# Kernel optimization log

Measured on AMD Instinct MI355X. Metric: run time of the kernel, lower is better.

## Reference

```python
import jax, jax.numpy as jnp
import numpy as np

EMBED = 1024
HEAD = 64
BLOCK = 2048
B = 8


def setup_inputs() -> dict:
    key = jax.random.key(0)
    k1, k2, k3, k4 = jax.random.split(key, 4)
    inputs = jax.random.normal(k1, (B, BLOCK, EMBED), dtype=jnp.float32)
    s = 1.0 / np.sqrt(EMBED)
    Wk = jax.random.normal(k2, (EMBED, HEAD), dtype=jnp.float32) * s
    Wq = jax.random.normal(k3, (EMBED, HEAD), dtype=jnp.float32) * s
    Wv = jax.random.normal(k4, (EMBED, HEAD), dtype=jnp.float32) * s
    return {"inputs": inputs, "Wk": Wk, "Wq": Wq, "Wv": Wv}


def reference(inputs, Wk, Wq, Wv):
    # inputs: [B, T, E]; projections (bias-free Linear)
    k = inputs @ Wk  # [B, T, H]
    q = inputs @ Wq  # [B, T, H]
    v = inputs @ Wv  # [B, T, H]
    # Faithful to source: wei = k @ q^T (NOT q @ k^T)
    wei = jnp.einsum("bth,bsh->bts", k, q) * (HEAD ** -0.5)  # [B, T, T]
    T = inputs.shape[1]
    causal = jnp.tril(jnp.ones((T, T), dtype=bool))
    wei = jnp.where(causal, wei, -jnp.inf)
    wei = jax.nn.softmax(wei, axis=-1)
    out = jnp.einsum("bts,bsh->bth", wei, v)  # [B, T, H]
    return out
```

## Files before the change

### kernel.cpp

```cpp
#include <hip/hip_runtime.h>
#include <hip/hip_bf16.h>
#include <stdint.h>


typedef __attribute__((ext_vector_type(4))) float f32x4;
typedef __attribute__((ext_vector_type(4))) short s16x4;
typedef __attribute__((ext_vector_type(8))) short s16x8;
typedef __attribute__((ext_vector_type(2))) unsigned int u32x2;
typedef __attribute__((ext_vector_type(4))) unsigned int u32x4;

__device__ __forceinline__ unsigned bf16pack(float a, float b){
    unsigned ua = __builtin_bit_cast(unsigned, a);
    unsigned ub = __builtin_bit_cast(unsigned, b);
    return ((ua + 0x8000u) >> 16) | ((ub + 0x8000u) & 0xffff0000u);
}
__device__ __forceinline__ unsigned short bf16one(float a){
    return (unsigned short)((__builtin_bit_cast(unsigned, a) + 0x8000u) >> 16);
}
__device__ __forceinline__ void gload16(const void* g, unsigned short* l){
    __builtin_amdgcn_global_load_lds((const __attribute__((address_space(1))) unsigned int*)g,
                                     (__attribute__((address_space(3))) unsigned int*)l, 16, 0, 0);
}

__global__ __launch_bounds__(256) void wprep_kernel(const float* __restrict__ Wk,
                                                    const float* __restrict__ Wq,
                                                    const float* __restrict__ Wv,
                                                    unsigned short* __restrict__ WT){
    __shared__ float lw[1024][8];
    int w = blockIdx.x, n0 = blockIdx.y * 8, tid = threadIdx.x;
    const float* src = (w == 0) ? Wk : (w == 1) ? Wq : Wv;
    float scale = (w == 0) ? 0.18033688011112042f : 1.0f;
    for (int it = 0; it < 8; ++it){
        int idx = it * 256 + tid;
        int k = idx >> 1, half = idx & 1;
        f32x4 v = *(const f32x4*)(src + k * 64 + n0 + half * 4);
        *(f32x4*)&lw[k][half * 4] = v;
    }
    __syncthreads();
    int n = tid >> 5, kc = (tid & 31) * 32;
    unsigned short* dst = WT + (size_t)((w * 64 + n0 + n) * 1024 + kc);
    #pragma unroll
    for (int c = 0; c < 4; c++){
        s16x8 v;
        #pragma unroll
        for (int e = 0; e < 8; e++)
            v[e] = (short)bf16one(lw[kc + c * 8 + e][n] * scale);
        *(s16x8*)(dst + c * 8) = v;
    }
}

__global__ __launch_bounds__(256) void proj_kernel(const float* __restrict__ x,
                                                   const unsigned short* __restrict__ WT,
                                                   unsigned short* __restrict__ kb,
                                                   unsigned short* __restrict__ qb,
                                                   unsigned short* __restrict__ vT){
    __shared__ unsigned short smem[32768];
    int tid = threadIdx.x; int l = tid & 63; int w = tid >> 6;
    int lr = l & 15, lg = l >> 4;
    int row0 = blockIdx.x * 32;
    int b = row0 >> 11, t0 = row0 & 2047;
    const float* xbase = x + (size_t)row0 * 1024;

    auto stage = [&](int k0, int buf){
        #pragma unroll
        for (int t = 0; t < 2; t++){
            int i = w * 2 + t;
            int r = i * 4 + (l >> 4);
            int c = l & 15;
            gload16(xbase + (size_t)r * 1024 + k0 + ((c ^ ((r & 7) << 1)) * 4),
                    smem + buf * 4096 + i * 512);
        }
        #pragma unroll
        for (int u = 0; u < 6; u++){
            int i = w * 6 + u;
            int r = i * 8 + (l >> 3);
            int c = l & 7;
            gload16(WT + (size_t)r * 1024 + k0 + ((c ^ (r & 7)) * 8),
                    smem + 8192 + buf * 12288 + i * 512);
        }
    };

    f32x4 acc[2][3] = {};
    stage(0, 0);
    __syncthreads();
    int cur = 0;
    for (int k0 = 0; k0 < 1024; k0 += 64){
        int kn = (k0 + 64 < 1024) ? (k0 + 64) : 960;
        stage(kn, cur ^ 1);
        s16x8 af[2][2];
        #pragma unroll
        for (int mf = 0; mf < 2; mf++){
            int r = mf * 16 + lr;
            const unsigned short* xrow = smem + cur * 4096 + r * 128;
            #pragma unroll
            for (int kc = 0; kc < 2; kc++){
                int c0 = (kc * 8 + lg * 2) ^ ((r & 7) << 1);
                f32x4 v0 = *(const f32x4*)(xrow + c0 * 8);
                f32x4 v1 = *(const f32x4*)(xrow + c0 * 8 + 8);
                u32x4 pk;
                pk[0] = bf16pack(v0[0], v0[1]); pk[1] = bf16pack(v0[2], v0[3]);
                pk[2] = bf16pack(v1[0], v1[1]); pk[3] = bf16pack(v1[2], v1[3]);
                af[mf][kc] = __builtin_bit_cast(s16x8, pk);
            }
        }
        #pragma unroll
        for (int nn = 0; nn < 3; nn++){
            int r = (w * 3 + nn) * 16 + lr;
            const unsigned short* wrow = smem + 8192 + cur * 12288 + r * 64;
            s16x8 b0 = *(const s16x8*)(wrow + ((lg       ^ (r & 7)) * 8));
            s16x8 b1 = *(const s16x8*)(wrow + (((4 + lg) ^ (r & 7)) * 8));
            acc[0][nn] = __builtin_amdgcn_mfma_f32_16x16x32_bf16(af[0][0], b0, acc[0][nn], 0, 0, 0);
            acc[0][nn] = __builtin_amdgcn_mfma_f32_16x16x32_bf16(af[0][1], b1, acc[0][nn], 0, 0, 0);
            acc[1][nn] = __builtin_amdgcn_mfma_f32_16x16x32_bf16(af[1][0], b0, acc[1][nn], 0, 0, 0);
            acc[1][nn] = __builtin_amdgcn_mfma_f32_16x16x32_bf16(af[1][1], b1, acc[1][nn], 0, 0, 0);
        }
        __syncthreads();
        cur ^= 1;
    }
    #pragma unroll
    for (int mf = 0; mf < 2; mf++)
        #pragma unroll
        for (int nn = 0; nn < 3; nn++){
            int col = (w * 3 + nn) * 16 + lr;
            int row = mf * 16 + lg * 4;
            #pragma unroll
            for (int r = 0; r < 4; r++)
                smem[(row + r) * 200 + col] = bf16one(acc[mf][nn][r]);
        }
    __syncthreads();
    {
        int r2 = tid >> 3, c2 = (tid & 7) * 16;
        const unsigned short* srowp = smem + r2 * 200 + c2;
        unsigned short* dst = (c2 < 64)
            ? kb + (size_t)(b * 2048 + t0 + r2) * 64 + c2
            : qb + (size_t)(b * 2048 + t0 + r2) * 64 + (c2 - 64);
        *(s16x8*)(dst)     = *(const s16x8*)(srowp);
        *(s16x8*)(dst + 8) = *(const s16x8*)(srowp + 8);
        int h = tid >> 2, q3 = tid & 3;
        s16x8 vv;
        #pragma unroll
        for (int e = 0; e < 8; e++)
            vv[e] = smem[(q3 * 8 + e) * 200 + 128 + h];
        *(s16x8*)(vT + (size_t)(b * 64 + h) * 2048 + t0 + q3 * 8) = vv;
    }
}

template<int NS>
__global__ __launch_bounds__(256) void attn_part_kernel(const unsigned short* __restrict__ kb,
                                                        const unsigned short* __restrict__ qb,
                                                        const unsigned short* __restrict__ vT,
                                                        float* __restrict__ out,
                                                        float* __restrict__ accp,
                                                        float* __restrict__ ml){
    __shared__ unsigned short Klds[2][64 * 64];
    __shared__ unsigned short Vlds[2][64 * 64];
    int tid = threadIdx.x; int l = tid & 63; int w = tid >> 6;
    int lr = l & 15, lg = l >> 4;
    int bx = blockIdx.x;
    int b = bx & 7;
    int r9 = bx >> 3;
    int bt = 31 - (r9 / NS);
    int strip = r9 % NS;
    int t0 = bt * 64;
    int tw = t0 + w * 16;
    const unsigned short* fqp = kb + (size_t)(b * 2048 + tw + lr) * 64 + lg * 8;
    s16x8 fq0 = *(const s16x8*)(fqp);
    s16x8 fq1 = *(const s16x8*)(fqp + 32);
    const unsigned short* qbb = qb + (size_t)b * 2048 * 64;
    const unsigned short* vbb = vT + (size_t)b * 64 * 2048;

    int srhi = l >> 3;
    int schk = l & 7;
    f32x4 acc[4] = {};
    float mrun = -3.0e38f, lrun = 0.0f;

    {
        int s0 = strip * 64;
        #pragma unroll
        for (int t = 0; t < 2; t++){
            int ti = w * 2 + t;
            int row = ti * 8 + srhi;
            gload16(qbb + (size_t)(s0 + row) * 64 + ((schk ^ (row & 7)) * 8), &Klds[0][ti * 512]);
            gload16(vbb + (size_t)row * 2048 + s0 + ((schk ^ (row & 7)) * 8), &Vlds[0][ti * 512]);
        }
    }
    __syncthreads();
    int cur = 0;
    for (int c = strip; c <= bt; c += NS){
        int nc = (c + NS <= bt) ? (c + NS) : c;
        int ns0 = nc * 64;
        #pragma unroll
        for (int t = 0; t < 2; t++){
            int ti = w * 2 + t;
            int row = ti * 8 + srhi;
            gload16(qbb + (size_t)(ns0 + row) * 64 + ((schk ^ (row & 7)) * 8), &Klds[cur ^ 1][ti * 512]);
            gload16(vbb + (size_t)row * 2048 + ns0 + ((schk ^ (row & 7)) * 8), &Vlds[cur ^ 1][ti * 512]);
        }
        f32x4 Cs[4];
        #pragma unroll
        for (int n = 0; n < 4; n++){
            int r = n * 16 + lr;
            const unsigned short* ka = &Klds[cur][r * 64];
            s16x8 k0 = *(const s16x8*)(ka + ((lg       ^ (r & 7)) * 8));
            s16x8 k1 = *(const s16x8*)(ka + (((4 + lg) ^ (r & 7)) * 8));
            f32x4 z = {};
            z     = __builtin_amdgcn_mfma_f32_16x16x32_bf16(k0, fq0, z, 0, 0, 0);
            Cs[n] = __builtin_amdgcn_mfma_f32_16x16x32_bf16(k1, fq1, z, 0, 0, 0);
        }
        if (c == bt){
            #pragma unroll
            for (int n = 0; n < 4; n++)
                #pragma unroll
                for (int r = 0; r < 4; r++)
                    if (n * 16 + lg * 4 + r > w * 16 + lr) Cs[n][r] = -3.0e38f;
        }
        float pm = -3.0e38f;
        #pragma unroll
        for (int n = 0; n < 4; n++)
            #pragma unroll
            for (int r = 0; r < 4; r++) pm = fmaxf(pm, Cs[n][r]);
        pm = fmaxf(pm, __shfl_xor(pm, 16));
        pm = fmaxf(pm, __shfl_xor(pm, 32));
        float mnew = fmaxf(mrun, pm);
        float scl = exp2f(mrun - mnew);
        float p[4][4]; float ps = 0.0f;
        #pragma unroll
        for (int n = 0; n < 4; n++)
            #pragma unroll
            for (int r = 0; r < 4; r++){ float e = exp2f(Cs[n][r] - mnew); p[n][r] = e; ps += e; }
        ps += __shfl_xor(ps, 16);
        ps += __shfl_xor(ps, 32);
        lrun = lrun * scl + ps;
        mrun = mnew;
        #pragma unroll
        for (int h16 = 0; h16 < 4; h16++) acc[h16] *= scl;
        s16x4 pb[4];
        #pragma unroll
        for (int n = 0; n < 4; n++){
            u32x2 t; t[0] = bf16pack(p[n][0], p[n][1]); t[1] = bf16pack(p[n][2], p[n][3]);
            pb[n] = __builtin_bit_cast(s16x4, t);
        }
        #pragma unroll
        for (int h16 = 0; h16 < 4; h16++){
            int r = h16 * 16 + lr;
            const unsigned short* va = &Vlds[cur][r * 64];
            #pragma unroll
            for (int sl = 0; sl < 4; sl++){
                s16x4 fv = *(const s16x4*)(va + (((sl * 2 + (lg >> 1)) ^ (r & 7)) * 8) + (lg & 1) * 4);
                acc[h16] = __builtin_amdgcn_mfma_f32_16x16x16bf16_1k(fv, pb[sl], acc[h16], 0, 0, 0);
            }
        }
        __syncthreads();
        cur ^= 1;
    }
    float* accdst = (strip == 0) ? out : (accp + (size_t)(strip - 1) * (8 * 2048 * 64));
    #pragma unroll
    for (int h16 = 0; h16 < 4; h16++)
        *(f32x4*)(accdst + (size_t)(b * 2048 + tw + lr) * 64 + h16 * 16 + lg * 4) = acc[h16];
    if (lg == 0){
        int idx = ((strip * 8 + b) * 32 + bt) * 64 + w * 16 + lr;
        ml[idx * 2]     = mrun;
        ml[idx * 2 + 1] = lrun;
    }
}

template<int NS>
__global__ __launch_bounds__(256) void attn_merge_kernel(const float* __restrict__ accp,
                                                         const float* __restrict__ ml,
                                                         float* __restrict__ out){
    int bt = blockIdx.x, b = blockIdx.y;
    int tid = threadIdx.x;
    int row = tid >> 2, cg = (tid & 3) * 16;
    float m[NS], lv[NS];
    float mg = -3.0e38f;
    #pragma unroll
    for (int s = 0; s < NS; s++){
        int idx = (((s * 8 + b) * 32 + bt) * 64 + row) * 2;
        m[s] = ml[idx]; lv[s] = ml[idx + 1];
        mg = fmaxf(mg, m[s]);
    }
    float wt[NS]; float lt = 0.0f;
    #pragma unroll
    for (int s = 0; s < NS; s++){ wt[s] = exp2f(m[s] - mg); lt += lv[s] * wt[s]; }
    float inv = 1.0f / lt;
    size_t base = (size_t)(b * 2048 + bt * 64 + row) * 64 + cg;
    #pragma unroll
    for (int g = 0; g < 4; g++){
        f32x4 o = (*(const f32x4*)(out + base + g * 4)) * wt[0];
        #pragma unroll
        for (int s = 1; s < NS; s++)
            o += (*(const f32x4*)(accp + (size_t)(s - 1) * (8 * 2048 * 64) + base + g * 4)) * wt[s];
        o *= inv;
        *(f32x4*)(out + base + g * 4) = o;
    }
}

__global__ __launch_bounds__(256) void attn_kernel(const unsigned short* __restrict__ kb,
                                                   const unsigned short* __restrict__ qb,
                                                   const unsigned short* __restrict__ vT,
                                                   float* __restrict__ out){
    __shared__ unsigned short Klds[2][64 * 64];
    __shared__ unsigned short Vlds[2][64 * 64];
    int tid = threadIdx.x; int l = tid & 63; int w = tid >> 6;
    int lr = l & 15, lg = l >> 4;
    int bx = blockIdx.x;
    int b = bx & 7;
    int bt = bx >> 3;
    int t0 = bt * 64;
    int tw = t0 + w * 16;
    const unsigned short* fqp = kb + (size_t)(b * 2048 + tw + lr) * 64 + lg * 8;
    s16x8 fq0 = *(const s16x8*)(fqp);
    s16x8 fq1 = *(const s16x8*)(fqp + 32);
    const unsigned short* qbb = qb + (size_t)b * 2048 * 64;
    const unsigned short* vbb = vT + (size_t)b * 64 * 2048;
    int srhi = l >> 3;
    int schk = l & 7;
    f32x4 acc[4] = {};
    float mrun = -3.0e38f, lrun = 0.0f;
    #pragma unroll
    for (int t = 0; t < 2; t++){
        int ti = w * 2 + t;
        int row = ti * 8 + srhi;
        gload16(qbb + (size_t)row * 64 + ((schk ^ (row & 7)) * 8), &Klds[0][ti * 512]);
        gload16(vbb + (size_t)row * 2048 + ((schk ^ (row & 7)) * 8), &Vlds[0][ti * 512]);
    }
    __syncthreads();
    int cur = 0;
    for (int c = 0; c <= bt; ++c){
        int nc = (c + 1 <= bt) ? (c + 1) : bt;
        int ns0 = nc * 64;
        #pragma unroll
        for (int t = 0; t < 2; t++){
            int ti = w * 2 + t;
            int row = ti * 8 + srhi;
            gload16(qbb + (size_t)(ns0 + row) * 64 + ((schk ^ (row & 7)) * 8), &Klds[cur ^ 1][ti * 512]);
            gload16(vbb + (size_t)row * 2048 + ns0 + ((schk ^ (row & 7)) * 8), &Vlds[cur ^ 1][ti * 512]);
        }
        f32x4 Cs[4];
        #pragma unroll
        for (int n = 0; n < 4; n++){
            int r = n * 16 + lr;
            const unsigned short* ka = &Klds[cur][r * 64];
            s16x8 k0 = *(const s16x8*)(ka + ((lg       ^ (r & 7)) * 8));
            s16x8 k1 = *(const s16x8*)(ka + (((4 + lg) ^ (r & 7)) * 8));
            f32x4 z = {};
            z     = __builtin_amdgcn_mfma_f32_16x16x32_bf16(k0, fq0, z, 0, 0, 0);
            Cs[n] = __builtin_amdgcn_mfma_f32_16x16x32_bf16(k1, fq1, z, 0, 0, 0);
        }
        if (c == bt){
            #pragma unroll
            for (int n = 0; n < 4; n++)
                #pragma unroll
                for (int r = 0; r < 4; r++)
                    if (n * 16 + lg * 4 + r > w * 16 + lr) Cs[n][r] = -3.0e38f;
        }
        float pm = -3.0e38f;
        #pragma unroll
        for (int n = 0; n < 4; n++)
            #pragma unroll
            for (int r = 0; r < 4; r++) pm = fmaxf(pm, Cs[n][r]);
        pm = fmaxf(pm, __shfl_xor(pm, 16));
        pm = fmaxf(pm, __shfl_xor(pm, 32));
        float mnew = fmaxf(mrun, pm);
        float scl = exp2f(mrun - mnew);
        float p[4][4]; float ps = 0.0f;
        #pragma unroll
        for (int n = 0; n < 4; n++)
            #pragma unroll
            for (int r = 0; r < 4; r++){ float e = exp2f(Cs[n][r] - mnew); p[n][r] = e; ps += e; }
        ps += __shfl_xor(ps, 16);
        ps += __shfl_xor(ps, 32);
        lrun = lrun * scl + ps;
        mrun = mnew;
        #pragma unroll
        for (int h16 = 0; h16 < 4; h16++) acc[h16] *= scl;
        s16x4 pb[4];
        #pragma unroll
        for (int n = 0; n < 4; n++){
            u32x2 t; t[0] = bf16pack(p[n][0], p[n][1]); t[1] = bf16pack(p[n][2], p[n][3]);
            pb[n] = __builtin_bit_cast(s16x4, t);
        }
        #pragma unroll
        for (int h16 = 0; h16 < 4; h16++){
            int r = h16 * 16 + lr;
            const unsigned short* va = &Vlds[cur][r * 64];
            #pragma unroll
            for (int sl = 0; sl < 4; sl++){
                s16x4 fv = *(const s16x4*)(va + (((sl * 2 + (lg >> 1)) ^ (r & 7)) * 8) + (lg & 1) * 4);
                acc[h16] = __builtin_amdgcn_mfma_f32_16x16x16bf16_1k(fv, pb[sl], acc[h16], 0, 0, 0);
            }
        }
        __syncthreads();
        cur ^= 1;
    }
    float inv = 1.0f / lrun;
    #pragma unroll
    for (int h16 = 0; h16 < 4; h16++){
        f32x4 o = acc[h16] * inv;
        *(f32x4*)(out + (size_t)(b * 2048 + tw + lr) * 64 + h16 * 16 + lg * 4) = o;
    }
}

extern "C" void kernel_launch(void* const* d_in, const int* in_sizes, int n_in,
                              void* d_out, int out_size, void* d_ws, size_t ws_size,
                              hipStream_t stream) {
    const float* x  = (const float*)d_in[0];
    const float* Wk = (const float*)d_in[1];
    const float* Wq = (const float*)d_in[2];
    const float* Wv = (const float*)d_in[3];
    float* out = (float*)d_out;
    char* ws = (char*)d_ws;
    if (ws_size < (size_t)7 * 1024 * 1024) return;
    unsigned short* WT = (unsigned short*)(ws);
    unsigned short* kb = (unsigned short*)(ws + (1u << 20));
    unsigned short* qb = (unsigned short*)(ws + (3u << 20));
    unsigned short* vT = (unsigned short*)(ws + (5u << 20));
    hipLaunchKernelGGL(wprep_kernel, dim3(3, 8), dim3(256), 0, stream, Wk, Wq, Wv, WT);
    hipLaunchKernelGGL(proj_kernel, dim3(512), dim3(256), 0, stream, x, WT, kb, qb, vT);
    if (ws_size >= (size_t)20 * 1024 * 1024){
        float* accp = (float*)(ws + ((size_t)7 << 20));
        float* ml   = (float*)(ws + ((size_t)19 << 20));
        hipLaunchKernelGGL((attn_part_kernel<4>), dim3(1024), dim3(256), 0, stream,
                           kb, qb, vT, out, accp, ml);
        hipLaunchKernelGGL((attn_merge_kernel<4>), dim3(32, 8), dim3(256), 0, stream,
                           accp, ml, out);
    } else if (ws_size >= (size_t)12 * 1024 * 1024){
        float* accp = (float*)(ws + ((size_t)7 << 20));
        float* ml   = (float*)(ws + ((size_t)11 << 20));
        hipLaunchKernelGGL((attn_part_kernel<2>), dim3(512), dim3(256), 0, stream,
                           kb, qb, vT, out, accp, ml);
        hipLaunchKernelGGL((attn_merge_kernel<2>), dim3(32, 8), dim3(256), 0, stream,
                           accp, ml, out);
    } else {
        hipLaunchKernelGGL(attn_kernel, dim3(256), dim3(256), 0, stream, kb, qb, vT, out);
    }
}
```

Measured before the change: 50.21 us.

## Enlarge projection tile to 64 rows and stage x as pre-packed bf16

The projection kernel now uses 512-thread blocks over 64 rows, half as many blocks, so each staged W tile is reused across twice as many rows. Each wave handles one 16-row slice and half of the 192 output columns. The x tile is no longer copied as fp32 through global_load_lds. Each thread loads 8 floats into registers during the current k-step, converts them to bf16, and writes them into the other LDS buffer. This cuts x LDS traffic and moves the bf16 conversion out of the MFMA loop. The cost is a register round trip on the x loads that is only partly overlapped, and fewer blocks (256) to fill the GPU.

After: 53.02 us. 5.6% more time.

```diff
diff --git a/kernel.cpp b/kernel.cpp
--- a/kernel.cpp
+++ b/kernel.cpp
@@ -49,7 +49,7 @@
     }
 }
 
-__global__ __launch_bounds__(256) void proj_kernel(const float* __restrict__ x,
+__global__ __launch_bounds__(512) void proj_kernel(const float* __restrict__ x,
                                                    const unsigned short* __restrict__ WT,
                                                    unsigned short* __restrict__ kb,
                                                    unsigned short* __restrict__ qb,
@@ -57,76 +57,71 @@
     __shared__ unsigned short smem[32768];
     int tid = threadIdx.x; int l = tid & 63; int w = tid >> 6;
     int lr = l & 15, lg = l >> 4;
-    int row0 = blockIdx.x * 32;
+    int mf = w >> 1, nh = w & 1;
+    int row0 = blockIdx.x * 64;
     int b = row0 >> 11, t0 = row0 & 2047;
     const float* xbase = x + (size_t)row0 * 1024;
 
-    auto stage = [&](int k0, int buf){
-        #pragma unroll
-        for (int t = 0; t < 2; t++){
-            int i = w * 2 + t;
-            int r = i * 4 + (l >> 4);
-            int c = l & 15;
-            gload16(xbase + (size_t)r * 1024 + k0 + ((c ^ ((r & 7) << 1)) * 4),
-                    smem + buf * 4096 + i * 512);
-        }
-        #pragma unroll
-        for (int u = 0; u < 6; u++){
-            int i = w * 6 + u;
+    int sr = tid >> 3, sc = tid & 7;
+    const float* sg = xbase + (size_t)sr * 1024 + sc * 8;
+    unsigned short* swr = smem + sr * 64 + ((sc ^ (sr & 7)) * 8);
+
+    auto stageW = [&](int k0, int buf){
+        #pragma unroll
+        for (int u = 0; u < 3; u++){
+            int i = w * 3 + u;
             int r = i * 8 + (l >> 3);
             int c = l & 7;
             gload16(WT + (size_t)r * 1024 + k0 + ((c ^ (r & 7)) * 8),
                     smem + 8192 + buf * 12288 + i * 512);
         }
     };
-
-    f32x4 acc[2][3] = {};
-    stage(0, 0);
+    auto xpack = [&](const f32x4& a, const f32x4& b2){
+        u32x4 pk;
+        pk[0] = bf16pack(a[0], a[1]);  pk[1] = bf16pack(a[2], a[3]);
+        pk[2] = bf16pack(b2[0], b2[1]); pk[3] = bf16pack(b2[2], b2[3]);
+        return pk;
+    };
+
+    f32x4 acc[6] = {};
+
+    f32x4 xa0 = *(const f32x4*)(sg);
+    f32x4 xa1 = *(const f32x4*)(sg + 4);
+    *(u32x4*)swr = xpack(xa0, xa1);
+    stageW(0, 0);
     __syncthreads();
     int cur = 0;
     for (int k0 = 0; k0 < 1024; k0 += 64){
         int kn = (k0 + 64 < 1024) ? (k0 + 64) : 960;
-        stage(kn, cur ^ 1);
-        s16x8 af[2][2];
-        #pragma unroll
-        for (int mf = 0; mf < 2; mf++){
-            int r = mf * 16 + lr;
-            const unsigned short* xrow = smem + cur * 4096 + r * 128;
-            #pragma unroll
-            for (int kc = 0; kc < 2; kc++){
-                int c0 = (kc * 8 + lg * 2) ^ ((r & 7) << 1);
-                f32x4 v0 = *(const f32x4*)(xrow + c0 * 8);
-                f32x4 v1 = *(const f32x4*)(xrow + c0 * 8 + 8);
-                u32x4 pk;
-                pk[0] = bf16pack(v0[0], v0[1]); pk[1] = bf16pack(v0[2], v0[3]);
-                pk[2] = bf16pack(v1[0], v1[1]); pk[3] = bf16pack(v1[2], v1[3]);
-                af[mf][kc] = __builtin_bit_cast(s16x8, pk);
-            }
-        }
-        #pragma unroll
-        for (int nn = 0; nn < 3; nn++){
-            int r = (w * 3 + nn) * 16 + lr;
+        stageW(kn, cur ^ 1);
+        xa0 = *(const f32x4*)(sg + kn);
+        xa1 = *(const f32x4*)(sg + kn + 4);
+        s16x8 af[2];
+        int ar = mf * 16 + lr;
+        #pragma unroll
+        for (int kc = 0; kc < 2; kc++)
+            af[kc] = *(const s16x8*)(smem + cur * 4096 + ar * 64 + (((kc * 4 + lg) ^ (ar & 7)) * 8));
+        #pragma unroll
+        for (int nn = 0; nn < 6; nn++){
+            int r = (nh * 6 + nn) * 16 + lr;
             const unsigned short* wrow = smem + 8192 + cur * 12288 + r * 64;
             s16x8 b0 = *(const s16x8*)(wrow + ((lg       ^ (r & 7)) * 8));
             s16x8 b1 = *(const s16x8*)(wrow + (((4 + lg) ^ (r & 7)) * 8));
-            acc[0][nn] = __builtin_amdgcn_mfma_f32_16x16x32_bf16(af[0][0], b0, acc[0][nn], 0, 0, 0);
-            acc[0][nn] = __builtin_amdgcn_mfma_f32_16x16x32_bf16(af[0][1], b1, acc[0][nn], 0, 0, 0);
-            acc[1][nn] = __builtin_amdgcn_mfma_f32_16x16x32_bf16(af[1][0], b0, acc[1][nn], 0, 0, 0);
-            acc[1][nn] = __builtin_amdgcn_mfma_f32_16x16x32_bf16(af[1][1], b1, acc[1][nn], 0, 0, 0);
-        }
+            acc[nn] = __builtin_amdgcn_mfma_f32_16x16x32_bf16(af[0], b0, acc[nn], 0, 0, 0);
+            acc[nn] = __builtin_amdgcn_mfma_f32_16x16x32_bf16(af[1], b1, acc[nn], 0, 0, 0);
+        }
+        *(u32x4*)(swr + (cur ^ 1) * 4096) = xpack(xa0, xa1);
         __syncthreads();
         cur ^= 1;
     }
     #pragma unroll
-    for (int mf = 0; mf < 2; mf++)
-        #pragma unroll
-        for (int nn = 0; nn < 3; nn++){
-            int col = (w * 3 + nn) * 16 + lr;
-            int row = mf * 16 + lg * 4;
-            #pragma unroll
-            for (int r = 0; r < 4; r++)
-                smem[(row + r) * 200 + col] = bf16one(acc[mf][nn][r]);
-        }
+    for (int nn = 0; nn < 6; nn++){
+        int col = (nh * 6 + nn) * 16 + lr;
+        int row = mf * 16 + lg * 4;
+        #pragma unroll
+        for (int r = 0; r < 4; r++)
+            smem[(row + r) * 200 + col] = bf16one(acc[nn][r]);
+    }
     __syncthreads();
     {
         int r2 = tid >> 3, c2 = (tid & 7) * 16;
@@ -136,7 +131,7 @@
             : qb + (size_t)(b * 2048 + t0 + r2) * 64 + (c2 - 64);
         *(s16x8*)(dst)     = *(const s16x8*)(srowp);
         *(s16x8*)(dst + 8) = *(const s16x8*)(srowp + 8);
-        int h = tid >> 2, q3 = tid & 3;
+        int h = tid >> 3, q3 = tid & 7;
         s16x8 vv;
         #pragma unroll
         for (int e = 0; e < 8; e++)
@@ -416,7 +411,7 @@
     unsigned short* qb = (unsigned short*)(ws + (3u << 20));
     unsigned short* vT = (unsigned short*)(ws + (5u << 20));
     hipLaunchKernelGGL(wprep_kernel, dim3(3, 8), dim3(256), 0, stream, Wk, Wq, Wv, WT);
-    hipLaunchKernelGGL(proj_kernel, dim3(512), dim3(256), 0, stream, x, WT, kb, qb, vT);
+    hipLaunchKernelGGL(proj_kernel, dim3(256), dim3(512), 0, stream, x, WT, kb, qb, vT);
     if (ws_size >= (size_t)20 * 1024 * 1024){
         float* accp = (float*)(ws + ((size_t)7 << 20));
         float* ml   = (float*)(ws + ((size_t)19 << 20));
```

## Triple-buffer K/V LDS staging with partial vmcnt waits in attention partial kernel

Applied to the files above, without the earlier changes.

Moves the attention partial kernel from a double-buffered to a triple-buffered LDS pipeline. K/V tiles are now prefetched two iterations ahead. The full __syncthreads is replaced by an s_waitcnt vmcnt(4) plus a raw barrier, so the newest loads can stay in flight across iterations. This is meant to hide global-load latency better. The cost is 50% more LDS per block, which may reduce occupancy, and a few redundant clamped loads at the tail.

New measurement: 50.79 us. Within noise of the previous version (+1.2%).

```diff
diff --git a/kernel.cpp b/kernel.cpp
--- a/kernel.cpp
+++ b/kernel.cpp
@@ -152,8 +152,8 @@
                                                         float* __restrict__ out,
                                                         float* __restrict__ accp,
                                                         float* __restrict__ ml){
-    __shared__ unsigned short Klds[2][64 * 64];
-    __shared__ unsigned short Vlds[2][64 * 64];
+    __shared__ unsigned short Klds[3][64 * 64];
+    __shared__ unsigned short Vlds[3][64 * 64];
     int tid = threadIdx.x; int l = tid & 63; int w = tid >> 6;
     int lr = l & 15, lg = l >> 4;
     int bx = blockIdx.x;
@@ -173,61 +173,63 @@
     int schk = l & 7;
     f32x4 acc[4] = {};
     float mrun = -3.0e38f, lrun = 0.0f;
-
-    {
-        int s0 = strip * 64;
+    int n = (strip <= bt) ? ((bt - strip) / NS + 1) : 0;
+
+    auto stageC = [&](int i, int buf){
+        int ci = strip + i * NS;
+        int cc = (ci <= bt) ? ci : bt;
+        int s0 = cc * 64;
         #pragma unroll
         for (int t = 0; t < 2; t++){
             int ti = w * 2 + t;
             int row = ti * 8 + srhi;
-            gload16(qbb + (size_t)(s0 + row) * 64 + ((schk ^ (row & 7)) * 8), &Klds[0][ti * 512]);
-            gload16(vbb + (size_t)row * 2048 + s0 + ((schk ^ (row & 7)) * 8), &Vlds[0][ti * 512]);
-        }
-    }
-    __syncthreads();
-    int cur = 0;
-    for (int c = strip; c <= bt; c += NS){
-        int nc = (c + NS <= bt) ? (c + NS) : c;
-        int ns0 = nc * 64;
-        #pragma unroll
-        for (int t = 0; t < 2; t++){
-            int ti = w * 2 + t;
-            int row = ti * 8 + srhi;
-            gload16(qbb + (size_t)(ns0 + row) * 64 + ((schk ^ (row & 7)) * 8), &Klds[cur ^ 1][ti * 512]);
-            gload16(vbb + (size_t)row * 2048 + ns0 + ((schk ^ (row & 7)) * 8), &Vlds[cur ^ 1][ti * 512]);
-        }
+            gload16(qbb + (size_t)(s0 + row) * 64 + ((schk ^ (row & 7)) * 8), &Klds[buf][ti * 512]);
+            gload16(vbb + (size_t)row * 2048 + s0 + ((schk ^ (row & 7)) * 8), &Vlds[buf][ti * 512]);
+        }
+    };
+
+    stageC(0, 0);
+    stageC(1, 1);
+    asm volatile("s_waitcnt vmcnt(4)" ::: "memory");
+    __builtin_amdgcn_s_barrier();
+    asm volatile("" ::: "memory");
+
+    for (int i = 0; i < n; ++i){
+        stageC(i + 2, (i + 2) % 3);
+        int c = strip + i * NS;
+        int cur = i % 3;
         f32x4 Cs[4];
         #pragma unroll
-        for (int n = 0; n < 4; n++){
-            int r = n * 16 + lr;
+        for (int nn = 0; nn < 4; nn++){
+            int r = nn * 16 + lr;
             const unsigned short* ka = &Klds[cur][r * 64];
             s16x8 k0 = *(const s16x8*)(ka + ((lg       ^ (r & 7)) * 8));
             s16x8 k1 = *(const s16x8*)(ka + (((4 + lg) ^ (r & 7)) * 8));
             f32x4 z = {};
-            z     = __builtin_amdgcn_mfma_f32_16x16x32_bf16(k0, fq0, z, 0, 0, 0);
-            Cs[n] = __builtin_amdgcn_mfma_f32_16x16x32_bf16(k1, fq1, z, 0, 0, 0);
+            z      = __builtin_amdgcn_mfma_f32_16x16x32_bf16(k0, fq0, z, 0, 0, 0);
+            Cs[nn] = __builtin_amdgcn_mfma_f32_16x16x32_bf16(k1, fq1, z, 0, 0, 0);
         }
         if (c == bt){
             #pragma unroll
-            for (int n = 0; n < 4; n++)
+            for (int nn = 0; nn < 4; nn++)
                 #pragma unroll
                 for (int r = 0; r < 4; r++)
-                    if (n * 16 + lg * 4 + r > w * 16 + lr) Cs[n][r] = -3.0e38f;
+                    if (nn * 16 + lg * 4 + r > w * 16 + lr) Cs[nn][r] = -3.0e38f;
         }
         float pm = -3.0e38f;
         #pragma unroll
-        for (int n = 0; n < 4; n++)
-            #pragma unroll
-            for (int r = 0; r < 4; r++) pm = fmaxf(pm, Cs[n][r]);
+        for (int nn = 0; nn < 4; nn++)
+            #pragma unroll
+            for (int r = 0; r < 4; r++) pm = fmaxf(pm, Cs[nn][r]);
         pm = fmaxf(pm, __shfl_xor(pm, 16));
         pm = fmaxf(pm, __shfl_xor(pm, 32));
         float mnew = fmaxf(mrun, pm);
         float scl = exp2f(mrun - mnew);
         float p[4][4]; float ps = 0.0f;
         #pragma unroll
-        for (int n = 0; n < 4; n++)
-            #pragma unroll
-            for (int r = 0; r < 4; r++){ float e = exp2f(Cs[n][r] - mnew); p[n][r] = e; ps += e; }
+        for (int nn = 0; nn < 4; nn++)
+            #pragma unroll
+            for (int r = 0; r < 4; r++){ float e = exp2f(Cs[nn][r] - mnew); p[nn][r] = e; ps += e; }
         ps += __shfl_xor(ps, 16);
         ps += __shfl_xor(ps, 32);
         lrun = lrun * scl + ps;
@@ -236,9 +238,9 @@
         for (int h16 = 0; h16 < 4; h16++) acc[h16] *= scl;
         s16x4 pb[4];
         #pragma unroll
-        for (int n = 0; n < 4; n++){
-            u32x2 t; t[0] = bf16pack(p[n][0], p[n][1]); t[1] = bf16pack(p[n][2], p[n][3]);
-            pb[n] = __builtin_bit_cast(s16x4, t);
+        for (int nn = 0; nn < 4; nn++){
+            u32x2 t; t[0] = bf16pack(p[nn][0], p[nn][1]); t[1] = bf16pack(p[nn][2], p[nn][3]);
+            pb[nn] = __builtin_bit_cast(s16x4, t);
         }
         #pragma unroll
         for (int h16 = 0; h16 < 4; h16++){
@@ -250,8 +252,9 @@
                 acc[h16] = __builtin_amdgcn_mfma_f32_16x16x16bf16_1k(fv, pb[sl], acc[h16], 0, 0, 0);
             }
         }
-        __syncthreads();
-        cur ^= 1;
+        asm volatile("s_waitcnt vmcnt(4)" ::: "memory");
+        __builtin_amdgcn_s_barrier();
+        asm volatile("" ::: "memory");
     }
     float* accdst = (strip == 0) ? out : (accp + (size_t)(strip - 1) * (8 * 2048 * 64));
     #pragma unroll
```

## Fuse split-KV merge into attention kernel via last-block atomic counter

Applied to the files above, without the earlier changes.

Removes the separate merge kernel launch. Each partial-attention block fences its outputs and bumps a per-tile atomic counter, and the last strip to finish for a (batch, row-tile) does the log-sum-exp merge in place. The counters are zeroed inside the weight-prep kernel, so no extra launch is needed. This saves one kernel launch and its tail, at the cost of fences, an atomic per block, and a serialized merge tail on the last-arriving block.

After: 192.0 us. 3.82x slower.

```diff
diff --git a/kernel.cpp b/kernel.cpp
--- a/kernel.cpp
+++ b/kernel.cpp
@@ -25,9 +25,11 @@
 __global__ __launch_bounds__(256) void wprep_kernel(const float* __restrict__ Wk,
                                                     const float* __restrict__ Wq,
                                                     const float* __restrict__ Wv,
-                                                    unsigned short* __restrict__ WT){
+                                                    unsigned short* __restrict__ WT,
+                                                    int* __restrict__ cnt){
     __shared__ float lw[1024][8];
     int w = blockIdx.x, n0 = blockIdx.y * 8, tid = threadIdx.x;
+    if (w == 0 && blockIdx.y == 0) cnt[tid] = 0;
     const float* src = (w == 0) ? Wk : (w == 1) ? Wq : Wv;
     float scale = (w == 0) ? 0.18033688011112042f : 1.0f;
     for (int it = 0; it < 8; ++it){
@@ -151,9 +153,11 @@
                                                         const unsigned short* __restrict__ vT,
                                                         float* __restrict__ out,
                                                         float* __restrict__ accp,
-                                                        float* __restrict__ ml){
+                                                        float* __restrict__ ml,
+                                                        int* __restrict__ cnt){
     __shared__ unsigned short Klds[2][64 * 64];
     __shared__ unsigned short Vlds[2][64 * 64];
+    __shared__ int lastflag;
     int tid = threadIdx.x; int l = tid & 63; int w = tid >> 6;
     int lr = l & 15, lg = l >> 4;
     int bx = blockIdx.x;
@@ -262,36 +266,38 @@
         ml[idx * 2]     = mrun;
         ml[idx * 2 + 1] = lrun;
     }
-}
-
-template<int NS>
-__global__ __launch_bounds__(256) void attn_merge_kernel(const float* __restrict__ accp,
-                                                         const float* __restrict__ ml,
-                                                         float* __restrict__ out){
-    int bt = blockIdx.x, b = blockIdx.y;
-    int tid = threadIdx.x;
-    int row = tid >> 2, cg = (tid & 3) * 16;
-    float m[NS], lv[NS];
-    float mg = -3.0e38f;
-    #pragma unroll
-    for (int s = 0; s < NS; s++){
-        int idx = (((s * 8 + b) * 32 + bt) * 64 + row) * 2;
-        m[s] = ml[idx]; lv[s] = ml[idx + 1];
-        mg = fmaxf(mg, m[s]);
-    }
-    float wt[NS]; float lt = 0.0f;
-    #pragma unroll
-    for (int s = 0; s < NS; s++){ wt[s] = exp2f(m[s] - mg); lt += lv[s] * wt[s]; }
-    float inv = 1.0f / lt;
-    size_t base = (size_t)(b * 2048 + bt * 64 + row) * 64 + cg;
-    #pragma unroll
-    for (int g = 0; g < 4; g++){
-        f32x4 o = (*(const f32x4*)(out + base + g * 4)) * wt[0];
-        #pragma unroll
-        for (int s = 1; s < NS; s++)
-            o += (*(const f32x4*)(accp + (size_t)(s - 1) * (8 * 2048 * 64) + base + g * 4)) * wt[s];
-        o *= inv;
-        *(f32x4*)(out + base + g * 4) = o;
+    __threadfence();
+    __syncthreads();
+    if (tid == 0){
+        int old = atomicAdd(&cnt[b * 32 + bt], 1);
+        lastflag = (old == NS - 1) ? 1 : 0;
+    }
+    __syncthreads();
+    if (lastflag){
+        __threadfence();
+        int row = tid >> 2, cg = (tid & 3) * 16;
+        float m[NS], lv[NS];
+        float mg = -3.0e38f;
+        #pragma unroll
+        for (int s = 0; s < NS; s++){
+            int idx = (((s * 8 + b) * 32 + bt) * 64 + row) * 2;
+            m[s] = ml[idx]; lv[s] = ml[idx + 1];
+            mg = fmaxf(mg, m[s]);
+        }
+        float wt[NS]; float lt = 0.0f;
+        #pragma unroll
+        for (int s = 0; s < NS; s++){ wt[s] = exp2f(m[s] - mg); lt += lv[s] * wt[s]; }
+        float inv = 1.0f / lt;
+        size_t base = (size_t)(b * 2048 + bt * 64 + row) * 64 + cg;
+        #pragma unroll
+        for (int g = 0; g < 4; g++){
+            f32x4 o = (*(const f32x4*)(out + base + g * 4)) * wt[0];
+            #pragma unroll
+            for (int s = 1; s < NS; s++)
+                o += (*(const f32x4*)(accp + (size_t)(s - 1) * (8 * 2048 * 64) + base + g * 4)) * wt[s];
+            o *= inv;
+            *(f32x4*)(out + base + g * 4) = o;
+        }
     }
 }
 
@@ -412,25 +418,22 @@
     char* ws = (char*)d_ws;
     if (ws_size < (size_t)7 * 1024 * 1024) return;
     unsigned short* WT = (unsigned short*)(ws);
+    int* cnt = (int*)(ws + 960u * 1024);
     unsigned short* kb = (unsigned short*)(ws + (1u << 20));
     unsigned short* qb = (unsigned short*)(ws + (3u << 20));
     unsigned short* vT = (unsigned short*)(ws + (5u << 20));
-    hipLaunchKernelGGL(wprep_kernel, dim3(3, 8), dim3(256), 0, stream, Wk, Wq, Wv, WT);
+    hipLaunchKernelGGL(wprep_kernel, dim3(3, 8), dim3(256), 0, stream, Wk, Wq, Wv, WT, cnt);
     hipLaunchKernelGGL(proj_kernel, dim3(512), dim3(256), 0, stream, x, WT, kb, qb, vT);
     if (ws_size >= (size_t)20 * 1024 * 1024){
         float* accp = (float*)(ws + ((size_t)7 << 20));
         float* ml   = (float*)(ws + ((size_t)19 << 20));
         hipLaunchKernelGGL((attn_part_kernel<4>), dim3(1024), dim3(256), 0, stream,
-                           kb, qb, vT, out, accp, ml);
-        hipLaunchKernelGGL((attn_merge_kernel<4>), dim3(32, 8), dim3(256), 0, stream,
-                           accp, ml, out);
+                           kb, qb, vT, out, accp, ml, cnt);
     } else if (ws_size >= (size_t)12 * 1024 * 1024){
         float* accp = (float*)(ws + ((size_t)7 << 20));
         float* ml   = (float*)(ws + ((size_t)11 << 20));
         hipLaunchKernelGGL((attn_part_kernel<2>), dim3(512), dim3(256), 0, stream,
-                           kb, qb, vT, out, accp, ml);
-        hipLaunchKernelGGL((attn_merge_kernel<2>), dim3(32, 8), dim3(256), 0, stream,
-                           accp, ml, out);
+                           kb, qb, vT, out, accp, ml, cnt);
     } else {
         hipLaunchKernelGGL(attn_kernel, dim3(256), dim3(256), 0, stream, kb, qb, vT, out);
     }
```
